# Kernel tuning notes

Measured on AMD Instinct MI355X. Metric: run time of the kernel, lower is better.

Reference implementation:

```python
import jax, jax.numpy as jnp
import numpy as np

B, M, D = 2048, 1024, 64
NEG_INF = -1e30


def setup_inputs() -> dict:
    key = jax.random.key(0)
    ks = jax.random.split(key, 12)
    s = 0.1  # small init scale for weights
    x = jax.random.normal(ks[0], (B, M, 4), dtype=jnp.float32)
    pad_mask = jax.random.bernoulli(ks[1], 0.1, (B, M))  # True = padded point
    return {
        "x": x,
        "pad_mask": pad_mask,
        "W_in": s * jax.random.normal(ks[2], (4, D), dtype=jnp.float32),
        "b_in": jnp.zeros((D,), jnp.float32),
        "seed": s * jax.random.normal(ks[3], (D,), dtype=jnp.float32),
        "Wq": s * jax.random.normal(ks[4], (D, D), dtype=jnp.float32),
        "Wk": s * jax.random.normal(ks[5], (D, D), dtype=jnp.float32),
        "Wv": s * jax.random.normal(ks[6], (D, D), dtype=jnp.float32),
        "Wo": s * jax.random.normal(ks[7], (D, D), dtype=jnp.float32),
        "b_o": jnp.zeros((D,), jnp.float32),
        "w_loc": s * jax.random.normal(ks[8], (D + 4, 1), dtype=jnp.float32),
        "b_loc": jnp.zeros((1,), jnp.float32),
        "prelu_a": jnp.full((1,), 0.25, jnp.float32),  # PReLU default slope
    }


def _wnet_global(x, pad_mask, W_in, b_in, seed, Wq, Wk, Wv, Wo, b_o):
    # Set-transformer style attention pooling -> one embedding per set [B, D]
    h = x @ W_in + b_in                                  # [B, M, D]
    q = seed @ Wq                                        # [D]
    k = h @ Wk                                           # [B, M, D]
    v = h @ Wv                                           # [B, M, D]
    scores = jnp.einsum("d,bmd->bm", q, k) / jnp.sqrt(jnp.float32(D))
    scores = jnp.where(pad_mask, NEG_INF, scores)
    attn = jax.nn.softmax(scores, axis=-1)               # [B, M]
    pooled = jnp.einsum("bm,bmd->bd", attn, v)           # [B, D]
    return pooled @ Wo + b_o                             # [B, D]


def reference(x, pad_mask, W_in, b_in, seed, Wq, Wk, Wv, Wo, b_o, w_loc, b_loc, prelu_a):
    feat = _wnet_global(x, pad_mask, W_in, b_in, seed, Wq, Wk, Wv, Wo, b_o)  # [B, D]
    # WNet_local: Linear on concat([x, feat]) split into two matmuls (same math,
    # avoids materializing the [B, M, D+4] concat)
    z = x @ w_loc[:4] + (feat @ w_loc[4:])[:, None, :] + b_loc               # [B, M, 1]
    w = jnp.where(z >= 0, z, prelu_a * z)[..., 0]                            # PReLU, [B, M]
    w = jnp.where(pad_mask, 0.0, w)
    # WLS: A = [-los, 1], r = residuals; diag(w) @ A == w[...,None] * A
    A = jnp.concatenate([-x[:, :, 1:4], jnp.ones((B, M, 1), x.dtype)], axis=-1)  # [B, M, 4]
    r = x[:, :, 0:1]                                                             # [B, M, 1]
    WA = w[:, :, None] * A
    Wr = w[:, :, None] * r
    out = (jnp.linalg.pinv(WA) @ Wr)[..., 0]                                     # [B, 4]
    return out
```

## Files before the change

### kernel.cpp

```cpp
#include <hip/hip_runtime.h>
#include <math.h>

#define BB 2048
#define MM 1024
#define DD 64
#define NEG_INF_F (-1e30f)

__device__ __forceinline__ float wredsum(float v) {
#pragma unroll
  for (int o = 32; o > 0; o >>= 1) v += __shfl_down(v, o);
  return v;
}
__device__ __forceinline__ float wredmax(float v) {
#pragma unroll
  for (int o = 32; o > 0; o >>= 1) v = fmaxf(v, __shfl_down(v, o));
  return v;
}

__global__ __launch_bounds__(256) void wls_fused(
    const float* __restrict__ x,
    const int*   __restrict__ pad,
    const float* __restrict__ W_in,
    const float* __restrict__ b_in,
    const float* __restrict__ seed,
    const float* __restrict__ Wq,
    const float* __restrict__ Wk,
    const float* __restrict__ Wv,
    const float* __restrict__ Wo,
    const float* __restrict__ b_o,
    const float* __restrict__ w_loc,
    const float* __restrict__ b_loc,
    const float* __restrict__ prelu_a,
    float* __restrict__ out)
{
  const int tid  = threadIdx.x;
  const int b    = blockIdx.x;
  const int wave = tid >> 6;
  const int lane = tid & 63;

  __shared__ float qv[DD], kqv[DD], tv[DD], uv[DD];
  __shared__ float cst[10];
  __shared__ float rbuf[4][16];
  __shared__ float bcast[8];

  const float4* x4 = (const float4*)(x + (size_t)b * MM * 4);
  float4 xr[4];
  int mk[4];
#pragma unroll
  for (int k2 = 0; k2 < 4; ++k2) {
    xr[k2] = x4[tid + 256 * k2];
    mk[k2] = pad[(size_t)b * MM + tid + 256 * k2];
  }

  if (wave == 0) {
    float acc = 0.f;
    for (int e = 0; e < DD; ++e) acc += seed[e] * Wq[e * DD + lane];
    qv[lane] = acc;
  } else if (wave == 1) {
    float acc = 0.f;
    for (int j = 0; j < DD; ++j) acc += Wo[lane * DD + j] * w_loc[4 + j];
    tv[lane] = acc;
  }
  __syncthreads();
  if (wave == 0) {
    float acc = 0.f;
    for (int d = 0; d < DD; ++d) acc += Wk[lane * DD + d] * qv[d];
    kqv[lane] = acc;
  } else if (wave == 1) {
    float acc = 0.f;
    for (int j = 0; j < DD; ++j) acc += Wv[lane * DD + j] * tv[j];
    uv[lane] = acc;
  }
  __syncthreads();
  if (tid < 4) {
    float acc = 0.f;
    for (int e = 0; e < DD; ++e) acc += W_in[tid * DD + e] * kqv[e];
    cst[tid] = acc;
  } else if (tid == 4) {
    float acc = 0.f;
    for (int e = 0; e < DD; ++e) acc += b_in[e] * kqv[e];
    cst[4] = acc;
  } else if (tid >= 5 && tid < 9) {
    float acc = 0.f;
    for (int e = 0; e < DD; ++e) acc += W_in[(tid - 5) * DD + e] * uv[e];
    cst[tid] = acc;
  } else if (tid == 9) {
    float acc = 0.f;
    for (int e = 0; e < DD; ++e) acc += b_in[e] * uv[e] + b_o[e] * w_loc[4 + e];
    cst[9] = acc + b_loc[0];
  }
  __syncthreads();

  const float c40 = cst[0], c41 = cst[1], c42 = cst[2], c43 = cst[3], c0 = cst[4];
  const float d40 = cst[5], d41 = cst[6], d42 = cst[7], d43 = cst[8], d0 = cst[9];

  float sc[4];
  float pmax = -INFINITY;
#pragma unroll
  for (int k2 = 0; k2 < 4; ++k2) {
    float s = (xr[k2].x * c40 + xr[k2].y * c41 + xr[k2].z * c42 + xr[k2].w * c43 + c0) * 0.125f;
    if (mk[k2]) s = NEG_INF_F;
    sc[k2] = s;
    pmax = fmaxf(pmax, s);
  }
  pmax = wredmax(pmax);
  if (lane == 0) rbuf[wave][0] = pmax;
  __syncthreads();
  const float smax = fmaxf(fmaxf(rbuf[0][0], rbuf[1][0]), fmaxf(rbuf[2][0], rbuf[3][0]));
  __syncthreads();

  float se = 0.f, sx0 = 0.f, sx1 = 0.f, sx2 = 0.f, sx3 = 0.f;
#pragma unroll
  for (int k2 = 0; k2 < 4; ++k2) {
    float e = expf(sc[k2] - smax);
    se += e;
    sx0 += e * xr[k2].x; sx1 += e * xr[k2].y; sx2 += e * xr[k2].z; sx3 += e * xr[k2].w;
  }
  {
    float v5[5] = {se, sx0, sx1, sx2, sx3};
#pragma unroll
    for (int j = 0; j < 5; ++j) {
      float r = wredsum(v5[j]);
      if (lane == 0) rbuf[wave][j] = r;
    }
  }
  __syncthreads();
  if (tid < 5) bcast[tid] = rbuf[0][tid] + rbuf[1][tid] + rbuf[2][tid] + rbuf[3][tid];
  __syncthreads();

  const float Z = bcast[0];
  const float xb0 = bcast[1] / Z, xb1 = bcast[2] / Z, xb2 = bcast[3] / Z, xb3 = bcast[4] / Z;
  const float sB = xb0 * d40 + xb1 * d41 + xb2 * d42 + xb3 * d43 + d0;

  const float aP = prelu_a[0];
  const float wl0 = w_loc[0], wl1 = w_loc[1], wl2 = w_loc[2], wl3 = w_loc[3];

  float g0 = 0.f, g1 = 0.f, g2 = 0.f, g3 = 0.f, g4 = 0.f, g5 = 0.f, g6 = 0.f,
        g7 = 0.f, g8 = 0.f, g9 = 0.f, r0 = 0.f, r1 = 0.f, r2 = 0.f, r3 = 0.f;
#pragma unroll
  for (int k2 = 0; k2 < 4; ++k2) {
    const float x0 = xr[k2].x, x1 = xr[k2].y, x2 = xr[k2].z, x3 = xr[k2].w;
    float z = x0 * wl0 + x1 * wl1 + x2 * wl2 + x3 * wl3 + sB;
    float w = (z >= 0.f) ? z : aP * z;
    if (mk[k2]) w = 0.f;
    const float w2 = w * w;
    g0 += w2 * x1 * x1; g1 += w2 * x1 * x2; g2 += w2 * x1 * x3; g3 -= w2 * x1;
    g4 += w2 * x2 * x2; g5 += w2 * x2 * x3; g6 -= w2 * x2;
    g7 += w2 * x3 * x3; g8 -= w2 * x3;
    g9 += w2;
    r0 -= w2 * x1 * x0; r1 -= w2 * x2 * x0; r2 -= w2 * x3 * x0; r3 += w2 * x0;
  }
  {
    float vals[14] = {g0, g1, g2, g3, g4, g5, g6, g7, g8, g9, r0, r1, r2, r3};
#pragma unroll
    for (int j = 0; j < 14; ++j) {
      float r = wredsum(vals[j]);
      if (lane == 0) rbuf[wave][j] = r;
    }
  }
  __syncthreads();

  if (tid == 0) {
    double s14[14];
#pragma unroll
    for (int j = 0; j < 14; ++j)
      s14[j] = (double)rbuf[0][j] + (double)rbuf[1][j] +
               (double)rbuf[2][j] + (double)rbuf[3][j];
    double G[4][5];
    G[0][0] = s14[0]; G[0][1] = s14[1]; G[0][2] = s14[2]; G[0][3] = s14[3]; G[0][4] = s14[10];
    G[1][0] = s14[1]; G[1][1] = s14[4]; G[1][2] = s14[5]; G[1][3] = s14[6]; G[1][4] = s14[11];
    G[2][0] = s14[2]; G[2][1] = s14[5]; G[2][2] = s14[7]; G[2][3] = s14[8]; G[2][4] = s14[12];
    G[3][0] = s14[3]; G[3][1] = s14[6]; G[3][2] = s14[8]; G[3][3] = s14[9]; G[3][4] = s14[13];

    for (int c = 0; c < 4; ++c) {
      int p = c; double mv = fabs(G[c][c]);
      for (int rr = c + 1; rr < 4; ++rr)
        if (fabs(G[rr][c]) > mv) { mv = fabs(G[rr][c]); p = rr; }
      if (p != c)
        for (int j = c; j < 5; ++j) { double t = G[c][j]; G[c][j] = G[p][j]; G[p][j] = t; }
      const double inv = 1.0 / G[c][c];
      for (int rr = c + 1; rr < 4; ++rr) {
        const double f = G[rr][c] * inv;
        for (int j = c; j < 5; ++j) G[rr][j] -= f * G[c][j];
      }
    }
    double y[4];
    for (int c = 3; c >= 0; --c) {
      double acc = G[c][4];
      for (int j = c + 1; j < 4; ++j) acc -= G[c][j] * y[j];
      y[c] = acc / G[c][c];
    }
    float4 o;
    o.x = (float)y[0]; o.y = (float)y[1]; o.z = (float)y[2]; o.w = (float)y[3];
    *(float4*)(out + (size_t)b * 4) = o;
  }
}

extern "C" void kernel_launch(void* const* d_in, const int* in_sizes, int n_in,
                              void* d_out, int out_size, void* d_ws, size_t ws_size,
                              hipStream_t stream) {
  const float* x       = (const float*)d_in[0];
  const int*   pad     = (const int*)d_in[1];
  const float* W_in    = (const float*)d_in[2];
  const float* b_in    = (const float*)d_in[3];
  const float* seed    = (const float*)d_in[4];
  const float* Wq      = (const float*)d_in[5];
  const float* Wk      = (const float*)d_in[6];
  const float* Wv      = (const float*)d_in[7];
  const float* Wo      = (const float*)d_in[8];
  const float* b_o     = (const float*)d_in[9];
  const float* w_loc   = (const float*)d_in[10];
  const float* b_loc   = (const float*)d_in[11];
  const float* prelu_a = (const float*)d_in[12];
  float* out = (float*)d_out;

  wls_fused<<<dim3(BB), dim3(256), 0, stream>>>(
      x, pad, W_in, b_in, seed, Wq, Wk, Wv, Wo, b_o, w_loc, b_loc, prelu_a, out);
}
```

Before: 132.3 us.

## Hoist weight-constant folding into a separate kernel and map one wave per set

The weight-only reductions (seed·Wq·Wk, Wo·w_loc·Wv, folding with W_in) move out of every block into a single-block precompute kernel that writes ten constants to workspace. The main kernel now gives each set to one 64-lane wave, holding 16 points per lane, so all reductions become shuffle-only and every __syncthreads and shared-memory exchange is gone. It also uses __expf and folds the softmax normalisation into one reciprocal. The trade-offs are an extra kernel launch with a dependency between the two, higher register pressure from the 16-point register arrays, and a serial double-precision solve run by one lane per wave.

Measured after the change: 117.5 us. 1.13x faster.

```diff
diff --git a/kernel.cpp b/kernel.cpp
--- a/kernel.cpp
+++ b/kernel.cpp
@@ -6,143 +6,127 @@
 #define DD 64
 #define NEG_INF_F (-1e30f)
 
-__device__ __forceinline__ float wredsum(float v) {
-#pragma unroll
-  for (int o = 32; o > 0; o >>= 1) v += __shfl_down(v, o);
-  return v;
-}
-__device__ __forceinline__ float wredmax(float v) {
-#pragma unroll
-  for (int o = 32; o > 0; o >>= 1) v = fmaxf(v, __shfl_down(v, o));
-  return v;
-}
-
-__global__ __launch_bounds__(256) void wls_fused(
-    const float* __restrict__ x,
-    const int*   __restrict__ pad,
-    const float* __restrict__ W_in,
-    const float* __restrict__ b_in,
-    const float* __restrict__ seed,
-    const float* __restrict__ Wq,
-    const float* __restrict__ Wk,
-    const float* __restrict__ Wv,
-    const float* __restrict__ Wo,
-    const float* __restrict__ b_o,
-    const float* __restrict__ w_loc,
-    const float* __restrict__ b_loc,
-    const float* __restrict__ prelu_a,
-    float* __restrict__ out)
+__global__ __launch_bounds__(128) void consts_kernel(
+    const float* __restrict__ W_in, const float* __restrict__ b_in,
+    const float* __restrict__ seed, const float* __restrict__ Wq,
+    const float* __restrict__ Wk,   const float* __restrict__ Wv,
+    const float* __restrict__ Wo,   const float* __restrict__ b_o,
+    const float* __restrict__ w_loc, const float* __restrict__ b_loc,
+    float* __restrict__ cst)
 {
-  const int tid  = threadIdx.x;
-  const int b    = blockIdx.x;
-  const int wave = tid >> 6;
-  const int lane = tid & 63;
-
   __shared__ float qv[DD], kqv[DD], tv[DD], uv[DD];
-  __shared__ float cst[10];
-  __shared__ float rbuf[4][16];
-  __shared__ float bcast[8];
-
-  const float4* x4 = (const float4*)(x + (size_t)b * MM * 4);
-  float4 xr[4];
-  int mk[4];
-#pragma unroll
-  for (int k2 = 0; k2 < 4; ++k2) {
-    xr[k2] = x4[tid + 256 * k2];
-    mk[k2] = pad[(size_t)b * MM + tid + 256 * k2];
-  }
+  const int tid = threadIdx.x, wave = tid >> 6, lane = tid & 63;
 
   if (wave == 0) {
-    float acc = 0.f;
-    for (int e = 0; e < DD; ++e) acc += seed[e] * Wq[e * DD + lane];
-    qv[lane] = acc;
-  } else if (wave == 1) {
-    float acc = 0.f;
-    for (int j = 0; j < DD; ++j) acc += Wo[lane * DD + j] * w_loc[4 + j];
-    tv[lane] = acc;
+    float a = 0.f;
+#pragma unroll
+    for (int e = 0; e < DD; ++e) a += seed[e] * Wq[e * DD + lane];
+    qv[lane] = a;
+  } else {
+    float a = 0.f;
+#pragma unroll
+    for (int j = 0; j < DD; ++j) a += Wo[lane * DD + j] * w_loc[4 + j];
+    tv[lane] = a;
   }
   __syncthreads();
   if (wave == 0) {
-    float acc = 0.f;
-    for (int d = 0; d < DD; ++d) acc += Wk[lane * DD + d] * qv[d];
-    kqv[lane] = acc;
-  } else if (wave == 1) {
-    float acc = 0.f;
-    for (int j = 0; j < DD; ++j) acc += Wv[lane * DD + j] * tv[j];
-    uv[lane] = acc;
+    float a = 0.f;
+#pragma unroll
+    for (int d = 0; d < DD; ++d) a += Wk[lane * DD + d] * qv[d];
+    kqv[lane] = a;
+  } else {
+    float a = 0.f;
+#pragma unroll
+    for (int j = 0; j < DD; ++j) a += Wv[lane * DD + j] * tv[j];
+    uv[lane] = a;
   }
   __syncthreads();
   if (tid < 4) {
-    float acc = 0.f;
-    for (int e = 0; e < DD; ++e) acc += W_in[tid * DD + e] * kqv[e];
-    cst[tid] = acc;
+    float a = 0.f;
+#pragma unroll
+    for (int e = 0; e < DD; ++e) a += W_in[tid * DD + e] * kqv[e];
+    cst[tid] = a;
   } else if (tid == 4) {
-    float acc = 0.f;
-    for (int e = 0; e < DD; ++e) acc += b_in[e] * kqv[e];
-    cst[4] = acc;
+    float a = 0.f;
+#pragma unroll
+    for (int e = 0; e < DD; ++e) a += b_in[e] * kqv[e];
+    cst[4] = a;
   } else if (tid >= 5 && tid < 9) {
-    float acc = 0.f;
-    for (int e = 0; e < DD; ++e) acc += W_in[(tid - 5) * DD + e] * uv[e];
-    cst[tid] = acc;
+    float a = 0.f;
+#pragma unroll
+    for (int e = 0; e < DD; ++e) a += W_in[(tid - 5) * DD + e] * uv[e];
+    cst[tid] = a;
   } else if (tid == 9) {
-    float acc = 0.f;
-    for (int e = 0; e < DD; ++e) acc += b_in[e] * uv[e] + b_o[e] * w_loc[4 + e];
-    cst[9] = acc + b_loc[0];
+    float a = 0.f;
+#pragma unroll
+    for (int e = 0; e < DD; ++e) a += b_in[e] * uv[e] + b_o[e] * w_loc[4 + e];
+    cst[9] = a + b_loc[0];
   }
-  __syncthreads();
+}
+
+__global__ __launch_bounds__(256) void wls_wave(
+    const float* __restrict__ x,
+    const int*   __restrict__ pad,
+    const float* __restrict__ w_loc,
+    const float* __restrict__ prelu_a,
+    const float* __restrict__ cst,
+    float* __restrict__ out)
+{
+  const int lane = threadIdx.x & 63;
+  const int wv   = threadIdx.x >> 6;
+  const int b    = (blockIdx.x << 2) | wv;
 
   const float c40 = cst[0], c41 = cst[1], c42 = cst[2], c43 = cst[3], c0 = cst[4];
   const float d40 = cst[5], d41 = cst[6], d42 = cst[7], d43 = cst[8], d0 = cst[9];
+  const float wl0 = w_loc[0], wl1 = w_loc[1], wl2 = w_loc[2], wl3 = w_loc[3];
+  const float aP  = prelu_a[0];
 
-  float sc[4];
+  const float4* x4 = (const float4*)(x + (size_t)b * (MM * 4));
+  const int*    pd = pad + (size_t)b * MM;
+
+  float4 xr[16];
+  int    mk[16];
+#pragma unroll
+  for (int r = 0; r < 16; ++r) xr[r] = x4[lane + (r << 6)];
+#pragma unroll
+  for (int r = 0; r < 16; ++r) mk[r] = pd[lane + (r << 6)];
+
+  float sc[16];
   float pmax = -INFINITY;
 #pragma unroll
-  for (int k2 = 0; k2 < 4; ++k2) {
-    float s = (xr[k2].x * c40 + xr[k2].y * c41 + xr[k2].z * c42 + xr[k2].w * c43 + c0) * 0.125f;
-    if (mk[k2]) s = NEG_INF_F;
-    sc[k2] = s;
+  for (int r = 0; r < 16; ++r) {
+    float s = (xr[r].x * c40 + xr[r].y * c41 + xr[r].z * c42 + xr[r].w * c43 + c0) * 0.125f;
+    s = mk[r] ? NEG_INF_F : s;
+    sc[r] = s;
     pmax = fmaxf(pmax, s);
   }
-  pmax = wredmax(pmax);
-  if (lane == 0) rbuf[wave][0] = pmax;
-  __syncthreads();
-  const float smax = fmaxf(fmaxf(rbuf[0][0], rbuf[1][0]), fmaxf(rbuf[2][0], rbuf[3][0]));
-  __syncthreads();
+#pragma unroll
+  for (int o = 32; o > 0; o >>= 1) pmax = fmaxf(pmax, __shfl_xor(pmax, o));
 
   float se = 0.f, sx0 = 0.f, sx1 = 0.f, sx2 = 0.f, sx3 = 0.f;
 #pragma unroll
-  for (int k2 = 0; k2 < 4; ++k2) {
-    float e = expf(sc[k2] - smax);
+  for (int r = 0; r < 16; ++r) {
+    const float e = __expf(sc[r] - pmax);
     se += e;
-    sx0 += e * xr[k2].x; sx1 += e * xr[k2].y; sx2 += e * xr[k2].z; sx3 += e * xr[k2].w;
+    sx0 += e * xr[r].x; sx1 += e * xr[r].y; sx2 += e * xr[r].z; sx3 += e * xr[r].w;
   }
-  {
-    float v5[5] = {se, sx0, sx1, sx2, sx3};
 #pragma unroll
-    for (int j = 0; j < 5; ++j) {
-      float r = wredsum(v5[j]);
-      if (lane == 0) rbuf[wave][j] = r;
-    }
+  for (int o = 32; o > 0; o >>= 1) {
+    se  += __shfl_xor(se, o);
+    sx0 += __shfl_xor(sx0, o); sx1 += __shfl_xor(sx1, o);
+    sx2 += __shfl_xor(sx2, o); sx3 += __shfl_xor(sx3, o);
   }
-  __syncthreads();
-  if (tid < 5) bcast[tid] = rbuf[0][tid] + rbuf[1][tid] + rbuf[2][tid] + rbuf[3][tid];
-  __syncthreads();
-
-  const float Z = bcast[0];
-  const float xb0 = bcast[1] / Z, xb1 = bcast[2] / Z, xb2 = bcast[3] / Z, xb3 = bcast[4] / Z;
-  const float sB = xb0 * d40 + xb1 * d41 + xb2 * d42 + xb3 * d43 + d0;
-
-  const float aP = prelu_a[0];
-  const float wl0 = w_loc[0], wl1 = w_loc[1], wl2 = w_loc[2], wl3 = w_loc[3];
+  const float invZ = 1.f / se;
+  const float sB = (sx0 * d40 + sx1 * d41 + sx2 * d42 + sx3 * d43) * invZ + d0;
 
   float g0 = 0.f, g1 = 0.f, g2 = 0.f, g3 = 0.f, g4 = 0.f, g5 = 0.f, g6 = 0.f,
         g7 = 0.f, g8 = 0.f, g9 = 0.f, r0 = 0.f, r1 = 0.f, r2 = 0.f, r3 = 0.f;
 #pragma unroll
-  for (int k2 = 0; k2 < 4; ++k2) {
-    const float x0 = xr[k2].x, x1 = xr[k2].y, x2 = xr[k2].z, x3 = xr[k2].w;
+  for (int r = 0; r < 16; ++r) {
+    const float x0 = xr[r].x, x1 = xr[r].y, x2 = xr[r].z, x3 = xr[r].w;
     float z = x0 * wl0 + x1 * wl1 + x2 * wl2 + x3 * wl3 + sB;
     float w = (z >= 0.f) ? z : aP * z;
-    if (mk[k2]) w = 0.f;
+    w = mk[r] ? 0.f : w;
     const float w2 = w * w;
     g0 += w2 * x1 * x1; g1 += w2 * x1 * x2; g2 += w2 * x1 * x3; g3 -= w2 * x1;
     g4 += w2 * x2 * x2; g5 += w2 * x2 * x3; g6 -= w2 * x2;
@@ -150,27 +134,19 @@
     g9 += w2;
     r0 -= w2 * x1 * x0; r1 -= w2 * x2 * x0; r2 -= w2 * x3 * x0; r3 += w2 * x0;
   }
-  {
-    float vals[14] = {g0, g1, g2, g3, g4, g5, g6, g7, g8, g9, r0, r1, r2, r3};
+  float vals[14] = {g0, g1, g2, g3, g4, g5, g6, g7, g8, g9, r0, r1, r2, r3};
 #pragma unroll
-    for (int j = 0; j < 14; ++j) {
-      float r = wredsum(vals[j]);
-      if (lane == 0) rbuf[wave][j] = r;
-    }
+  for (int j = 0; j < 14; ++j) {
+#pragma unroll
+    for (int o = 32; o > 0; o >>= 1) vals[j] += __shfl_down(vals[j], o);
   }
-  __syncthreads();
 
-  if (tid == 0) {
-    double s14[14];
-#pragma unroll
-    for (int j = 0; j < 14; ++j)
-      s14[j] = (double)rbuf[0][j] + (double)rbuf[1][j] +
-               (double)rbuf[2][j] + (double)rbuf[3][j];
+  if (lane == 0) {
     double G[4][5];
-    G[0][0] = s14[0]; G[0][1] = s14[1]; G[0][2] = s14[2]; G[0][3] = s14[3]; G[0][4] = s14[10];
-    G[1][0] = s14[1]; G[1][1] = s14[4]; G[1][2] = s14[5]; G[1][3] = s14[6]; G[1][4] = s14[11];
-    G[2][0] = s14[2]; G[2][1] = s14[5]; G[2][2] = s14[7]; G[2][3] = s14[8]; G[2][4] = s14[12];
-    G[3][0] = s14[3]; G[3][1] = s14[6]; G[3][2] = s14[8]; G[3][3] = s14[9]; G[3][4] = s14[13];
+    G[0][0] = vals[0]; G[0][1] = vals[1]; G[0][2] = vals[2]; G[0][3] = vals[3]; G[0][4] = vals[10];
+    G[1][0] = vals[1]; G[1][1] = vals[4]; G[1][2] = vals[5]; G[1][3] = vals[6]; G[1][4] = vals[11];
+    G[2][0] = vals[2]; G[2][1] = vals[5]; G[2][2] = vals[7]; G[2][3] = vals[8]; G[2][4] = vals[12];
+    G[3][0] = vals[3]; G[3][1] = vals[6]; G[3][2] = vals[8]; G[3][3] = vals[9]; G[3][4] = vals[13];
 
     for (int c = 0; c < 4; ++c) {
       int p = c; double mv = fabs(G[c][c]);
@@ -190,9 +166,9 @@
       for (int j = c + 1; j < 4; ++j) acc -= G[c][j] * y[j];
       y[c] = acc / G[c][c];
     }
-    float4 o;
-    o.x = (float)y[0]; o.y = (float)y[1]; o.z = (float)y[2]; o.w = (float)y[3];
-    *(float4*)(out + (size_t)b * 4) = o;
+    float4 o4;
+    o4.x = (float)y[0]; o4.y = (float)y[1]; o4.z = (float)y[2]; o4.w = (float)y[3];
+    *(float4*)(out + (size_t)b * 4) = o4;
   }
 }
 
@@ -213,7 +189,10 @@
   const float* b_loc   = (const float*)d_in[11];
   const float* prelu_a = (const float*)d_in[12];
   float* out = (float*)d_out;
+  float* cst = (float*)d_ws;
 
-  wls_fused<<<dim3(BB), dim3(256), 0, stream>>>(
-      x, pad, W_in, b_in, seed, Wq, Wk, Wv, Wo, b_o, w_loc, b_loc, prelu_a, out);
+  consts_kernel<<<dim3(1), dim3(128), 0, stream>>>(
+      W_in, b_in, seed, Wq, Wk, Wv, Wo, b_o, w_loc, b_loc, cst);
+  wls_wave<<<dim3(BB / 4), dim3(256), 0, stream>>>(
+      x, pad, w_loc, prelu_a, cst, out);
 }
```
